# Kernel tuning notes

Measured on AMD Instinct MI355X. Metric: run time of the kernel, lower is better.

## Reference

```python
import jax, jax.numpy as jnp
import numpy as np

N_HEADS = 4
DIM_HEAD = 32
SCALE = DIM_HEAD ** -0.5
EPS = 1e-5


def setup_inputs() -> dict:
    key = jax.random.key(0)
    ks = jax.random.split(key, 5)
    b, dim, l, h, w = 8, 128, 32, 32, 32
    hidden = N_HEADS * DIM_HEAD  # 128
    return {
        "x": jax.random.normal(ks[0], (b, dim, l, h, w), dtype=jnp.float32),
        "w_qkv": jax.random.normal(ks[1], (3 * hidden, dim), dtype=jnp.float32) * 0.05,
        "w_out": jax.random.normal(ks[2], (dim, hidden), dtype=jnp.float32) * 0.05,
        "b_out": jax.random.normal(ks[3], (dim,), dtype=jnp.float32) * 0.05,
        "gn_gamma": jnp.ones((dim,), dtype=jnp.float32),
        "gn_beta": jnp.zeros((dim,), dtype=jnp.float32),
    }


def reference(x, w_qkv, w_out, b_out, gn_gamma, gn_beta):
    b, dim, l, h_sp, w_sp = x.shape
    n = l * h_sp * w_sp
    hidden = N_HEADS * DIM_HEAD
    xf = x.reshape(b, dim, n)  # flatten spatial -> tokens
    # 1x1 conv == channel matmul: [3*hidden, dim] x [b, dim, n]
    qkv = jnp.einsum('oc,bcn->bon', w_qkv, xf)
    qkv = qkv.reshape(b, 3, N_HEADS, DIM_HEAD, n)
    q, k, v = qkv[:, 0], qkv[:, 1], qkv[:, 2]  # each [b, H, d, n]
    q = jax.nn.softmax(q, axis=2) * SCALE      # softmax over feature dim d
    k = jax.nn.softmax(k, axis=-1)             # softmax over tokens n
    c = jnp.einsum('bhdn,bhen->bhde', k, v)    # [b, H, d, e] tiny context
    out = jnp.einsum('bhde,bhdn->bhen', c, q)  # [b, H, e, n]
    out = out.reshape(b, hidden, n)
    # to_out 1x1 conv + bias
    y = jnp.einsum('oc,bcn->bon', w_out, out) + b_out[None, :, None]
    # GroupNorm(1, dim): normalize over (C, spatial) per sample
    mean = jnp.mean(y, axis=(1, 2), keepdims=True)
    var = jnp.var(y, axis=(1, 2), keepdims=True)
    y = (y - mean) * jax.lax.rsqrt(var + EPS)
    y = y * gn_gamma[None, :, None] + gn_beta[None, :, None]
    return y.reshape(b, dim, l, h_sp, w_sp)
```

## Files before the change

### kernel.cpp

```cpp
#include <hip/hip_runtime.h>

#define BATCH 8
#define DIMC 128
#define NTOT 32768
#define HEADS 4
#define DHEAD 32
#define SCALE_Q 0.17677669529663687f
#define GRIDX 128
#define TILES 4

typedef _Float16 half8  __attribute__((ext_vector_type(8)));
typedef _Float16 half4v __attribute__((ext_vector_type(4)));
typedef _Float16 half2v __attribute__((ext_vector_type(2)));
typedef float    f32x4  __attribute__((ext_vector_type(4)));

#define WS_WQKV 0
#define WS_WOUT 98304
#define WS_S    131072
#define WS_Z    262144
#define WS_ST   266240
#define WS_CT   266304
#define WS_NEED 331840

__global__ void k0_prep(const float* __restrict__ wqkv, const float* __restrict__ wout,
                        char* __restrict__ ws) {
    int i = blockIdx.x * 256 + threadIdx.x;
    _Float16* Wb = (_Float16*)(ws + WS_WQKV);
    _Float16* Wo = (_Float16*)(ws + WS_WOUT);
    float* S  = (float*)(ws + WS_S);
    float* Z  = (float*)(ws + WS_Z);
    float* St = (float*)(ws + WS_ST);
    if (i < 49152) Wb[i] = (_Float16)wqkv[i];
    int j = i - 49152;
    if (j >= 0 && j < 16384) Wo[j] = (_Float16)wout[j];
    int k = j - 16384;
    if (k >= 0 && k < 32768) S[k] = 0.f;
    int m = k - 32768;
    if (m >= 0 && m < 1024) Z[m] = 0.f;
    int s = m - 1024;
    if (s >= 0 && s < 16) St[s] = 0.f;
}

__global__ __launch_bounds__(256, 2) void k1_kv(const float* __restrict__ x,
                                                const _Float16* __restrict__ Wb,
                                                float* __restrict__ S,
                                                float* __restrict__ Z) {
    __shared__ _Float16 Xb[64][136];
    __shared__ _Float16 KB[128][64];
    __shared__ _Float16 VB[128][64];
    const int t = threadIdx.x;
    const int lane = t & 63, w = t >> 6, g = lane >> 4, l15 = lane & 15;
    const int b = blockIdx.y;

    half8 af[4][4];
#pragma unroll
    for (int mt = 0; mt < 4; ++mt)
#pragma unroll
        for (int kc = 0; kc < 4; ++kc)
            af[mt][kc] = *(const half8*)(Wb + (size_t)(128 + (w * 4 + mt) * 16 + l15) * 128 + kc * 32 + 8 * g);

    f32x4 sacc[2][2];
#pragma unroll
    for (int dm = 0; dm < 2; ++dm)
#pragma unroll
        for (int en = 0; en < 2; ++en) sacc[dm][en] = (f32x4){0.f, 0.f, 0.f, 0.f};
    float zpart = 0.f;

    const int j4 = t & 15, c0 = t >> 4;
    const int sxw = (j4 & 7) << 3;

    float4 xr[8];
#pragma unroll
    for (int cc = 0; cc < 8; ++cc)
        xr[cc] = *(const float4*)(x + ((size_t)b * DIMC + c0 + 16 * cc) * NTOT + blockIdx.x * 64 + 4 * j4);
#pragma unroll
    for (int cc = 0; cc < 8; ++cc) {
        const int c = c0 + 16 * cc;
        Xb[4 * j4 + 0][c ^ sxw] = (_Float16)xr[cc].x;
        Xb[4 * j4 + 1][c ^ sxw] = (_Float16)xr[cc].y;
        Xb[4 * j4 + 2][c ^ sxw] = (_Float16)xr[cc].z;
        Xb[4 * j4 + 3][c ^ sxw] = (_Float16)xr[cc].w;
    }

    for (int it = 0; it < TILES; ++it) {
        if (it < TILES - 1) {
            const int j0n = (blockIdx.x + GRIDX * (it + 1)) * 64;
#pragma unroll
            for (int cc = 0; cc < 8; ++cc)
                xr[cc] = *(const float4*)(x + ((size_t)b * DIMC + c0 + 16 * cc) * NTOT + j0n + 4 * j4);
        }
        __syncthreads();
        half8 bf[4][4];
#pragma unroll
        for (int nt = 0; nt < 4; ++nt) {
            const int sb = ((4 * nt + (l15 >> 2)) & 7) << 3;
#pragma unroll
            for (int kc = 0; kc < 4; ++kc)
                bf[nt][kc] = *(const half8*)(&Xb[nt * 16 + l15][(kc * 32 + 8 * g) ^ sb]);
        }
#pragma unroll
        for (int mt = 0; mt < 4; ++mt) {
            f32x4 a0 = (f32x4){0.f,0.f,0.f,0.f}, a1 = a0, a2 = a0, a3 = a0;
#pragma unroll
            for (int kc = 0; kc < 4; ++kc) {
                a0 = __builtin_amdgcn_mfma_f32_16x16x32_f16(af[mt][kc], bf[0][kc], a0, 0, 0, 0);
                a1 = __builtin_amdgcn_mfma_f32_16x16x32_f16(af[mt][kc], bf[1][kc], a1, 0, 0, 0);
                a2 = __builtin_amdgcn_mfma_f32_16x16x32_f16(af[mt][kc], bf[2][kc], a2, 0, 0, 0);
                a3 = __builtin_amdgcn_mfma_f32_16x16x32_f16(af[mt][kc], bf[3][kc], a3, 0, 0, 0);
            }
            const int lr0 = (w * 4 + mt) * 16 + g * 4;
            const int skv = (((w * 4 + mt) * 4 + g) & 7) << 3;
#pragma unroll
            for (int nt = 0; nt < 4; ++nt) {
                const f32x4 a = (nt == 0) ? a0 : (nt == 1) ? a1 : (nt == 2) ? a2 : a3;
                const int jn = (nt * 16 + l15) ^ skv;
                if (lr0 < 128) {
#pragma unroll
                    for (int r = 0; r < 4; ++r) KB[lr0 + r][jn] = (_Float16)__expf(a[r]);
                } else {
#pragma unroll
                    for (int r = 0; r < 4; ++r) VB[lr0 - 128 + r][jn] = (_Float16)a[r];
                }
            }
        }
        __syncthreads();
        if (it < TILES - 1) {
#pragma unroll
            for (int cc = 0; cc < 8; ++cc) {
                const int c = c0 + 16 * cc;
                Xb[4 * j4 + 0][c ^ sxw] = (_Float16)xr[cc].x;
                Xb[4 * j4 + 1][c ^ sxw] = (_Float16)xr[cc].y;
                Xb[4 * j4 + 2][c ^ sxw] = (_Float16)xr[cc].z;
                Xb[4 * j4 + 3][c ^ sxw] = (_Float16)xr[cc].w;
            }
        }
#pragma unroll
        for (int dm = 0; dm < 2; ++dm) {
            const int sr = ((4 * dm + (l15 >> 2)) & 7) << 3;
#pragma unroll
            for (int en = 0; en < 2; ++en)
#pragma unroll
                for (int kc = 0; kc < 2; ++kc) {
                    half8 ka = *(const half8*)(&KB[w * 32 + dm * 16 + l15][(kc * 32 + 8 * g) ^ sr]);
                    half8 vb = *(const half8*)(&VB[w * 32 + en * 16 + l15][(kc * 32 + 8 * g) ^ sr]);
                    sacc[dm][en] = __builtin_amdgcn_mfma_f32_16x16x32_f16(ka, vb, sacc[dm][en], 0, 0, 0);
                }
        }
        {
            const int zr = lane >> 1;
            const int sz = ((zr >> 2) & 7) << 3;
#pragma unroll
            for (int s8 = 0; s8 < 4; ++s8) {
                half8 hv = *(const half8*)(&KB[w * 32 + zr][((lane & 1) * 32 + 8 * s8) ^ sz]);
#pragma unroll
                for (int e = 0; e < 8; ++e) zpart += (float)hv[e];
            }
        }
    }
    {
        float zt = zpart + __shfl_xor(zpart, 1);
        if ((lane & 1) == 0) atomicAdd(&Z[(b * HEADS + w) * DHEAD + (lane >> 1)], zt);
    }
#pragma unroll
    for (int dm = 0; dm < 2; ++dm)
#pragma unroll
        for (int en = 0; en < 2; ++en)
#pragma unroll
            for (int r = 0; r < 4; ++r)
                atomicAdd(&S[((size_t)(b * HEADS + w) * DHEAD + dm * 16 + g * 4 + r) * DHEAD + en * 16 + l15],
                          sacc[dm][en][r]);
}

__global__ void k2_ct(const float* __restrict__ S, const float* __restrict__ Z,
                      _Float16* __restrict__ CT) {
    int i = blockIdx.x * 256 + threadIdx.x;
    int d = i & 31, e = (i >> 5) & 31, bh = i >> 10;
    CT[i] = (_Float16)(S[(bh * 32 + d) * 32 + e] / Z[bh * 32 + d]);
}

__global__ __launch_bounds__(256, 2) void k3_main(const float* __restrict__ x,
                                                  const _Float16* __restrict__ Wb,
                                                  const _Float16* __restrict__ Wo,
                                                  const _Float16* __restrict__ CT,
                                                  const float* __restrict__ b_out,
                                                  char* __restrict__ ybase,
                                                  float* __restrict__ St) {
    __shared__ _Float16 Xb[64][136];
    __shared__ _Float16 qT[64][136];
    __shared__ _Float16 oT[64][136];
    __shared__ float scl[4][64];
    __shared__ float red[8];
    const int t = threadIdx.x;
    const int lane = t & 63, w = t >> 6, g = lane >> 4, l15 = lane & 15;
    const int b = blockIdx.y;
    const int j4 = t & 15, c0 = t >> 4;
    const int sxw = (j4 & 7) << 3;

    half8 wa[2][4];
#pragma unroll
    for (int mi = 0; mi < 2; ++mi)
#pragma unroll
        for (int kc = 0; kc < 4; ++kc)
            wa[mi][kc] = *(const half8*)(Wb + (size_t)((w * 2 + mi) * 16 + l15) * 128 + kc * 32 + 8 * g);
    half8 ca[2];
#pragma unroll
    for (int et = 0; et < 2; ++et)
        ca[et] = *(const half8*)(CT + ((size_t)(b * HEADS + w) * DHEAD + et * 16 + l15) * DHEAD + 8 * g);

    float ssum = 0.f, ssq = 0.f;

    float4 xr[8];
#pragma unroll
    for (int cc = 0; cc < 8; ++cc)
        xr[cc] = *(const float4*)(x + ((size_t)b * DIMC + c0 + 16 * cc) * NTOT + blockIdx.x * 64 + 4 * j4);
#pragma unroll
    for (int cc = 0; cc < 8; ++cc) {
        const int c = c0 + 16 * cc;
        Xb[4 * j4 + 0][c ^ sxw] = (_Float16)xr[cc].x;
        Xb[4 * j4 + 1][c ^ sxw] = (_Float16)xr[cc].y;
        Xb[4 * j4 + 2][c ^ sxw] = (_Float16)xr[cc].z;
        Xb[4 * j4 + 3][c ^ sxw] = (_Float16)xr[cc].w;
    }
    __syncthreads();

    for (int it = 0; it < TILES; ++it) {
        const int j0 = (blockIdx.x + GRIDX * it) * 64;
        if (it < TILES - 1) {
            const int j0n = (blockIdx.x + GRIDX * (it + 1)) * 64;
#pragma unroll
            for (int cc = 0; cc < 8; ++cc)
                xr[cc] = *(const float4*)(x + ((size_t)b * DIMC + c0 + 16 * cc) * NTOT + j0n + 4 * j4);
        }
        {
            half8 bf[4][4];
#pragma unroll
            for (int nt = 0; nt < 4; ++nt) {
                const int sb = ((4 * nt + (l15 >> 2)) & 7) << 3;
#pragma unroll
                for (int kc = 0; kc < 4; ++kc)
                    bf[nt][kc] = *(const half8*)(&Xb[nt * 16 + l15][(kc * 32 + 8 * g) ^ sb]);
            }
            float ps[4] = {0.f, 0.f, 0.f, 0.f};
#pragma unroll
            for (int mi = 0; mi < 2; ++mi) {
                const int mt = w * 2 + mi;
                f32x4 acc[4];
#pragma unroll
                for (int nt = 0; nt < 4; ++nt) acc[nt] = (f32x4){0.f, 0.f, 0.f, 0.f};
#pragma unroll
                for (int kc = 0; kc < 4; ++kc)
#pragma unroll
                    for (int nt = 0; nt < 4; ++nt)
                        acc[nt] = __builtin_amdgcn_mfma_f32_16x16x32_f16(wa[mi][kc], bf[nt][kc], acc[nt], 0, 0, 0);
#pragma unroll
                for (int nt = 0; nt < 4; ++nt) {
                    const int sb = ((4 * nt + (l15 >> 2)) & 7) << 3;
                    half4v p;
#pragma unroll
                    for (int r = 0; r < 4; ++r) {
                        const float e = __expf(acc[nt][r]);
                        ps[nt] += e;
                        p[r] = (_Float16)e;
                    }
                    *(half4v*)(&qT[nt * 16 + l15][(mt * 16 + g * 4) ^ sb]) = p;
                }
            }
#pragma unroll
            for (int nt = 0; nt < 4; ++nt) {
                ps[nt] += __shfl_xor(ps[nt], 16);
                ps[nt] += __shfl_xor(ps[nt], 32);
            }
            if (lane < 16) {
#pragma unroll
                for (int nt = 0; nt < 4; ++nt) scl[w][nt * 16 + lane] = SCALE_Q / ps[nt];
            }
        }
        __syncthreads();
        if (it < TILES - 1) {
#pragma unroll
            for (int cc = 0; cc < 8; ++cc) {
                const int c = c0 + 16 * cc;
                Xb[4 * j4 + 0][c ^ sxw] = (_Float16)xr[cc].x;
                Xb[4 * j4 + 1][c ^ sxw] = (_Float16)xr[cc].y;
                Xb[4 * j4 + 2][c ^ sxw] = (_Float16)xr[cc].z;
                Xb[4 * j4 + 3][c ^ sxw] = (_Float16)xr[cc].w;
            }
        }
        {
            half8 bf3[4];
            float sc[4];
#pragma unroll
            for (int nt = 0; nt < 4; ++nt) {
                const int sb = ((4 * nt + (l15 >> 2)) & 7) << 3;
                bf3[nt] = *(const half8*)(&qT[nt * 16 + l15][(w * 32 + 8 * g) ^ sb]);
                sc[nt] = scl[w][nt * 16 + l15];
            }
#pragma unroll
            for (int et = 0; et < 2; ++et) {
                f32x4 acc[4];
#pragma unroll
                for (int nt = 0; nt < 4; ++nt) acc[nt] = (f32x4){0.f, 0.f, 0.f, 0.f};
#pragma unroll
                for (int nt = 0; nt < 4; ++nt)
                    acc[nt] = __builtin_amdgcn_mfma_f32_16x16x32_f16(ca[et], bf3[nt], acc[nt], 0, 0, 0);
#pragma unroll
                for (int nt = 0; nt < 4; ++nt) {
                    const int sb = ((4 * nt + (l15 >> 2)) & 7) << 3;
                    half4v p;
#pragma unroll
                    for (int r = 0; r < 4; ++r) p[r] = (_Float16)(acc[nt][r] * sc[nt]);
                    *(half4v*)(&oT[nt * 16 + l15][(w * 32 + et * 16 + g * 4) ^ sb]) = p;
                }
            }
        }
        __syncthreads();
        {
            half8 bf[4][4];
#pragma unroll
            for (int nt = 0; nt < 4; ++nt) {
                const int sb = ((4 * nt + (l15 >> 2)) & 7) << 3;
#pragma unroll
                for (int kc = 0; kc < 4; ++kc)
                    bf[nt][kc] = *(const half8*)(&oT[nt * 16 + l15][(kc * 32 + 8 * g) ^ sb]);
            }
#pragma unroll
            for (int mi = 0; mi < 2; ++mi) {
                const int mt = w * 2 + mi;
                const int o0 = mt * 16 + g * 4;
                half8 af[4];
#pragma unroll
                for (int kc = 0; kc < 4; ++kc)
                    af[kc] = *(const half8*)(Wo + (size_t)(mt * 16 + l15) * 128 + kc * 32 + 8 * g);
                f32x4 acc[4];
#pragma unroll
                for (int nt = 0; nt < 4; ++nt) acc[nt] = (f32x4){0.f, 0.f, 0.f, 0.f};
#pragma unroll
                for (int kc = 0; kc < 4; ++kc)
#pragma unroll
                    for (int nt = 0; nt < 4; ++nt)
                        acc[nt] = __builtin_amdgcn_mfma_f32_16x16x32_f16(af[kc], bf[nt][kc], acc[nt], 0, 0, 0);
                float bo[4];
#pragma unroll
                for (int r = 0; r < 4; ++r) bo[r] = b_out[o0 + r];
#pragma unroll
                for (int r = 0; r < 4; ++r) {
                    _Float16* yrow = (_Float16*)(ybase + (size_t)(b * DIMC + o0 + r) * 131072 + 65536);
#pragma unroll
                    for (int nt = 0; nt < 4; ++nt) {
                        const int jn = j0 + nt * 16 + l15;
                        const float yv = acc[nt][r] + bo[r];
                        ssum += yv;
                        ssq += yv * yv;
                        yrow[jn] = (_Float16)yv;
                    }
                }
            }
        }
        __syncthreads();
    }
#pragma unroll
    for (int m = 32; m; m >>= 1) { ssum += __shfl_xor(ssum, m); ssq += __shfl_xor(ssq, m); }
    if (lane == 0) { red[w] = ssum; red[4 + w] = ssq; }
    __syncthreads();
    if (t == 0) {
        atomicAdd(&St[b * 2 + 0], red[0] + red[1] + red[2] + red[3]);
        atomicAdd(&St[b * 2 + 1], red[4] + red[5] + red[6] + red[7]);
    }
}

__global__ __launch_bounds__(256) void k4_norm(float* __restrict__ out, const float* __restrict__ St,
                                               const float* __restrict__ gamma,
                                               const float* __restrict__ beta) {
    const int o = blockIdx.x;
    const int b = blockIdx.y;
    const int t = threadIdx.x;
    const size_t row = (size_t)b * DIMC + o;
    const float n = (float)DIMC * (float)NTOT;
    const float mean = St[b * 2] / n;
    const float var = St[b * 2 + 1] / n - mean * mean;
    const float rs = rsqrtf(var + 1e-5f);
    const float ga = gamma[o] * rs;
    const float be = beta[o];
    const half8* yh = (const half8*)((const char*)out + row * 131072 + 65536);
    half8 hbuf[16];
#pragma unroll
    for (int i = 0; i < 16; ++i) hbuf[i] = yh[i * 256 + t];
    __syncthreads();
    float4* orow = (float4*)(out + row * NTOT);
#pragma unroll
    for (int i = 0; i < 16; ++i) {
        const int e4 = (i * 256 + t) * 2;
        float4 v0, v1;
        v0.x = ((float)hbuf[i][0] - mean) * ga + be;
        v0.y = ((float)hbuf[i][1] - mean) * ga + be;
        v0.z = ((float)hbuf[i][2] - mean) * ga + be;
        v0.w = ((float)hbuf[i][3] - mean) * ga + be;
        v1.x = ((float)hbuf[i][4] - mean) * ga + be;
        v1.y = ((float)hbuf[i][5] - mean) * ga + be;
        v1.z = ((float)hbuf[i][6] - mean) * ga + be;
        v1.w = ((float)hbuf[i][7] - mean) * ga + be;
        orow[e4] = v0;
        orow[e4 + 1] = v1;
    }
}

extern "C" void kernel_launch(void* const* d_in, const int* in_sizes, int n_in,
                              void* d_out, int out_size, void* d_ws, size_t ws_size,
                              hipStream_t stream) {
    const float* x     = (const float*)d_in[0];
    const float* wqkv  = (const float*)d_in[1];
    const float* wout  = (const float*)d_in[2];
    const float* b_out = (const float*)d_in[3];
    const float* gamma = (const float*)d_in[4];
    const float* beta  = (const float*)d_in[5];
    if (ws_size < WS_NEED) return;
    char* ws = (char*)d_ws;
    _Float16* Wb = (_Float16*)(ws + WS_WQKV);
    _Float16* Wo = (_Float16*)(ws + WS_WOUT);
    float* S  = (float*)(ws + WS_S);
    float* Z  = (float*)(ws + WS_Z);
    float* St = (float*)(ws + WS_ST);
    _Float16* CT = (_Float16*)(ws + WS_CT);

    k0_prep<<<389, 256, 0, stream>>>(wqkv, wout, ws);
    k1_kv<<<dim3(GRIDX, 8), 256, 0, stream>>>(x, Wb, S, Z);
    k2_ct<<<128, 256, 0, stream>>>(S, Z, CT);
    k3_main<<<dim3(GRIDX, 8), 256, 0, stream>>>(x, Wb, Wo, CT, b_out, (char*)d_out, St);
    k4_norm<<<dim3(128, 8), 256, 0, stream>>>((float*)d_out, St, gamma, beta);
}
```

Baseline: 153.7 us.

## Transpose x staging to per-token scalar loads with packed LDS writes, halve grid

The global-to-LDS staging of x in both the KV and main kernels changes from float4 loads along tokens to scalar loads where each thread owns one token and four consecutive channels. The four channels are packed into a single 8-byte half4 LDS store instead of four scattered 2-byte stores. This is meant to cut LDS store instructions and bank conflicts, while global loads stay coalesced across a wave. The grid in x is also halved and per-block tiles doubled, which lowers block count and amortizes the weight-fragment loads but reduces parallelism to 512 blocks.

```diff
diff --git a/kernel.cpp b/kernel.cpp
--- a/kernel.cpp
+++ b/kernel.cpp
@@ -6,8 +6,8 @@
 #define HEADS 4
 #define DHEAD 32
 #define SCALE_Q 0.17677669529663687f
-#define GRIDX 128
-#define TILES 4
+#define GRIDX 64
+#define TILES 8
 
 typedef _Float16 half8  __attribute__((ext_vector_type(8)));
 typedef _Float16 half4v __attribute__((ext_vector_type(4)));
@@ -41,6 +41,7 @@
     if (s >= 0 && s < 16) St[s] = 0.f;
 }
 
+
 __global__ __launch_bounds__(256, 2) void k1_kv(const float* __restrict__ x,
                                                 const _Float16* __restrict__ Wb,
                                                 float* __restrict__ S,
@@ -66,20 +67,19 @@
         for (int en = 0; en < 2; ++en) sacc[dm][en] = (f32x4){0.f, 0.f, 0.f, 0.f};
     float zpart = 0.f;
 
-    const int j4 = t & 15, c0 = t >> 4;
-    const int sxw = (j4 & 7) << 3;
-
-    float4 xr[8];
+    const int jt = t & 63, cq4 = (t >> 6) * 4;
+    const int sxw = ((jt >> 2) & 7) << 3;
+
+    float xr[8][4];
 #pragma unroll
     for (int cc = 0; cc < 8; ++cc)
-        xr[cc] = *(const float4*)(x + ((size_t)b * DIMC + c0 + 16 * cc) * NTOT + blockIdx.x * 64 + 4 * j4);
+#pragma unroll
+        for (int r = 0; r < 4; ++r)
+            xr[cc][r] = x[((size_t)b * DIMC + cq4 + 16 * cc + r) * NTOT + blockIdx.x * 64 + jt];
 #pragma unroll
     for (int cc = 0; cc < 8; ++cc) {
-        const int c = c0 + 16 * cc;
-        Xb[4 * j4 + 0][c ^ sxw] = (_Float16)xr[cc].x;
-        Xb[4 * j4 + 1][c ^ sxw] = (_Float16)xr[cc].y;
-        Xb[4 * j4 + 2][c ^ sxw] = (_Float16)xr[cc].z;
-        Xb[4 * j4 + 3][c ^ sxw] = (_Float16)xr[cc].w;
+        half4v p = {(_Float16)xr[cc][0], (_Float16)xr[cc][1], (_Float16)xr[cc][2], (_Float16)xr[cc][3]};
+        *(half4v*)(&Xb[jt][(cq4 + 16 * cc) ^ sxw]) = p;
     }
 
     for (int it = 0; it < TILES; ++it) {
@@ -87,7 +87,9 @@
             const int j0n = (blockIdx.x + GRIDX * (it + 1)) * 64;
 #pragma unroll
             for (int cc = 0; cc < 8; ++cc)
-                xr[cc] = *(const float4*)(x + ((size_t)b * DIMC + c0 + 16 * cc) * NTOT + j0n + 4 * j4);
+#pragma unroll
+                for (int r = 0; r < 4; ++r)
+                    xr[cc][r] = x[((size_t)b * DIMC + cq4 + 16 * cc + r) * NTOT + j0n + jt];
         }
         __syncthreads();
         half8 bf[4][4];
@@ -127,11 +129,8 @@
         if (it < TILES - 1) {
 #pragma unroll
             for (int cc = 0; cc < 8; ++cc) {
-                const int c = c0 + 16 * cc;
-                Xb[4 * j4 + 0][c ^ sxw] = (_Float16)xr[cc].x;
-                Xb[4 * j4 + 1][c ^ sxw] = (_Float16)xr[cc].y;
-                Xb[4 * j4 + 2][c ^ sxw] = (_Float16)xr[cc].z;
-                Xb[4 * j4 + 3][c ^ sxw] = (_Float16)xr[cc].w;
+                half4v p = {(_Float16)xr[cc][0], (_Float16)xr[cc][1], (_Float16)xr[cc][2], (_Float16)xr[cc][3]};
+                *(half4v*)(&Xb[jt][(cq4 + 16 * cc) ^ sxw]) = p;
             }
         }
 #pragma unroll
@@ -193,8 +192,8 @@
     const int t = threadIdx.x;
     const int lane = t & 63, w = t >> 6, g = lane >> 4, l15 = lane & 15;
     const int b = blockIdx.y;
-    const int j4 = t & 15, c0 = t >> 4;
-    const int sxw = (j4 & 7) << 3;
+    const int jt = t & 63, cq4 = (t >> 6) * 4;
+    const int sxw = ((jt >> 2) & 7) << 3;
 
     half8 wa[2][4];
 #pragma unroll
@@ -209,17 +208,16 @@
 
     float ssum = 0.f, ssq = 0.f;
 
-    float4 xr[8];
+    float xr[8][4];
 #pragma unroll
     for (int cc = 0; cc < 8; ++cc)
-        xr[cc] = *(const float4*)(x + ((size_t)b * DIMC + c0 + 16 * cc) * NTOT + blockIdx.x * 64 + 4 * j4);
+#pragma unroll
+        for (int r = 0; r < 4; ++r)
+            xr[cc][r] = x[((size_t)b * DIMC + cq4 + 16 * cc + r) * NTOT + blockIdx.x * 64 + jt];
 #pragma unroll
     for (int cc = 0; cc < 8; ++cc) {
-        const int c = c0 + 16 * cc;
-        Xb[4 * j4 + 0][c ^ sxw] = (_Float16)xr[cc].x;
-        Xb[4 * j4 + 1][c ^ sxw] = (_Float16)xr[cc].y;
-        Xb[4 * j4 + 2][c ^ sxw] = (_Float16)xr[cc].z;
-        Xb[4 * j4 + 3][c ^ sxw] = (_Float16)xr[cc].w;
+        half4v p = {(_Float16)xr[cc][0], (_Float16)xr[cc][1], (_Float16)xr[cc][2], (_Float16)xr[cc][3]};
+        *(half4v*)(&Xb[jt][(cq4 + 16 * cc) ^ sxw]) = p;
     }
     __syncthreads();
 
@@ -229,7 +227,9 @@
             const int j0n = (blockIdx.x + GRIDX * (it + 1)) * 64;
 #pragma unroll
             for (int cc = 0; cc < 8; ++cc)
-                xr[cc] = *(const float4*)(x + ((size_t)b * DIMC + c0 + 16 * cc) * NTOT + j0n + 4 * j4);
+#pragma unroll
+                for (int r = 0; r < 4; ++r)
+                    xr[cc][r] = x[((size_t)b * DIMC + cq4 + 16 * cc + r) * NTOT + j0n + jt];
         }
         {
             half8 bf[4][4];
@@ -279,11 +279,8 @@
         if (it < TILES - 1) {
 #pragma unroll
             for (int cc = 0; cc < 8; ++cc) {
-                const int c = c0 + 16 * cc;
-                Xb[4 * j4 + 0][c ^ sxw] = (_Float16)xr[cc].x;
-                Xb[4 * j4 + 1][c ^ sxw] = (_Float16)xr[cc].y;
-                Xb[4 * j4 + 2][c ^ sxw] = (_Float16)xr[cc].z;
-                Xb[4 * j4 + 3][c ^ sxw] = (_Float16)xr[cc].w;
+                half4v p = {(_Float16)xr[cc][0], (_Float16)xr[cc][1], (_Float16)xr[cc][2], (_Float16)xr[cc][3]};
+                *(half4v*)(&Xb[jt][(cq4 + 16 * cc) ^ sxw]) = p;
             }
         }
         {
```

After: 155.0 us. Within noise of the previous version (+0.8%).

## Fold per-head context into output projection weights, removing a GEMM stage

Applied to the files above, without the earlier changes.

A new small kernel premultiplies the output projection weights by the normalized per-head context matrices, giving a per-batch fused weight matrix G stored in a scratch slot of the output buffer. The main kernel then does one 128x128 MFMA GEMM on the scaled softmax of q instead of a context GEMM plus an output GEMM, which drops one LDS buffer, one barrier stage and the fp16 rounding of the intermediate. The q-softmax scale is now applied in registers before the LDS store. The grid is also halved with twice as many tiles per block, which lowers parallelism but amortizes the per-block setup, including loading the G fragments.

```diff
diff --git a/kernel.cpp b/kernel.cpp
--- a/kernel.cpp
+++ b/kernel.cpp
@@ -6,39 +6,33 @@
 #define HEADS 4
 #define DHEAD 32
 #define SCALE_Q 0.17677669529663687f
-#define GRIDX 128
-#define TILES 4
+#define GRIDX 64
+#define TILES 8
 
 typedef _Float16 half8  __attribute__((ext_vector_type(8)));
 typedef _Float16 half4v __attribute__((ext_vector_type(4)));
-typedef _Float16 half2v __attribute__((ext_vector_type(2)));
 typedef float    f32x4  __attribute__((ext_vector_type(4)));
 
 #define WS_WQKV 0
-#define WS_WOUT 98304
-#define WS_S    131072
-#define WS_Z    262144
-#define WS_ST   266240
-#define WS_CT   266304
-#define WS_NEED 331840
-
-__global__ void k0_prep(const float* __restrict__ wqkv, const float* __restrict__ wout,
-                        char* __restrict__ ws) {
+#define WS_S    98304
+#define WS_Z    229376
+#define WS_ST   233472
+#define WS_NEED 233536
+
+
+__global__ void k0_prep(const float* __restrict__ wqkv, char* __restrict__ ws) {
     int i = blockIdx.x * 256 + threadIdx.x;
     _Float16* Wb = (_Float16*)(ws + WS_WQKV);
-    _Float16* Wo = (_Float16*)(ws + WS_WOUT);
     float* S  = (float*)(ws + WS_S);
     float* Z  = (float*)(ws + WS_Z);
     float* St = (float*)(ws + WS_ST);
     if (i < 49152) Wb[i] = (_Float16)wqkv[i];
     int j = i - 49152;
-    if (j >= 0 && j < 16384) Wo[j] = (_Float16)wout[j];
-    int k = j - 16384;
-    if (k >= 0 && k < 32768) S[k] = 0.f;
-    int m = k - 32768;
-    if (m >= 0 && m < 1024) Z[m] = 0.f;
-    int s = m - 1024;
-    if (s >= 0 && s < 16) St[s] = 0.f;
+    if (j >= 0 && j < 32768) S[j] = 0.f;
+    int k = j - 32768;
+    if (k >= 0 && k < 1024) Z[k] = 0.f;
+    int m = k - 1024;
+    if (m >= 0 && m < 16) St[m] = 0.f;
 }
 
 __global__ __launch_bounds__(256, 2) void k1_kv(const float* __restrict__ x,
@@ -171,24 +165,40 @@
                           sacc[dm][en][r]);
 }
 
-__global__ void k2_ct(const float* __restrict__ S, const float* __restrict__ Z,
-                      _Float16* __restrict__ CT) {
-    int i = blockIdx.x * 256 + threadIdx.x;
-    int d = i & 31, e = (i >> 5) & 31, bh = i >> 10;
-    CT[i] = (_Float16)(S[(bh * 32 + d) * 32 + e] / Z[bh * 32 + d]);
+__global__ __launch_bounds__(256) void k2_g(const float* __restrict__ S, const float* __restrict__ Z,
+                                            const float* __restrict__ wout, char* __restrict__ ybase) {
+    __shared__ float Sd[32][33];
+    const int h = blockIdx.x, b = blockIdx.y;
+    const int t = threadIdx.x;
+    const float* Sb = S + (size_t)(b * HEADS + h) * 1024;
+    const float* Zb = Z + (size_t)(b * HEADS + h) * 32;
+    for (int i = t; i < 1024; i += 256) {
+        int d = i >> 5;
+        Sd[d][i & 31] = Sb[i] / Zb[d];
+    }
+    __syncthreads();
+    const int o = t & 127, dh = (t >> 7) * 16;
+    float wrow[32];
+#pragma unroll
+    for (int e = 0; e < 32; ++e) wrow[e] = wout[o * 128 + h * 32 + e];
+    _Float16* Gb = (_Float16*)(ybase + (size_t)(b >> 1) * 131072 + (size_t)(b & 1) * 32768);
+#pragma unroll
+    for (int dd = 0; dd < 16; ++dd) {
+        const int d = dh + dd;
+        float acc = 0.f;
+#pragma unroll
+        for (int e = 0; e < 32; ++e) acc = fmaf(wrow[e], Sd[d][e], acc);
+        Gb[o * 128 + h * 32 + d] = (_Float16)acc;
+    }
 }
 
 __global__ __launch_bounds__(256, 2) void k3_main(const float* __restrict__ x,
                                                   const _Float16* __restrict__ Wb,
-                                                  const _Float16* __restrict__ Wo,
-                                                  const _Float16* __restrict__ CT,
                                                   const float* __restrict__ b_out,
                                                   char* __restrict__ ybase,
                                                   float* __restrict__ St) {
     __shared__ _Float16 Xb[64][136];
     __shared__ _Float16 qT[64][136];
-    __shared__ _Float16 oT[64][136];
-    __shared__ float scl[4][64];
     __shared__ float red[8];
     const int t = threadIdx.x;
     const int lane = t & 63, w = t >> 6, g = lane >> 4, l15 = lane & 15;
@@ -197,15 +207,15 @@
     const int sxw = (j4 & 7) << 3;
 
     half8 wa[2][4];
+    half8 ga[2][4];
+    const _Float16* Gb = (const _Float16*)(ybase + (size_t)(b >> 1) * 131072 + (size_t)(b & 1) * 32768);
 #pragma unroll
     for (int mi = 0; mi < 2; ++mi)
 #pragma unroll
-        for (int kc = 0; kc < 4; ++kc)
+        for (int kc = 0; kc < 4; ++kc) {
             wa[mi][kc] = *(const half8*)(Wb + (size_t)((w * 2 + mi) * 16 + l15) * 128 + kc * 32 + 8 * g);
-    half8 ca[2];
-#pragma unroll
-    for (int et = 0; et < 2; ++et)
-        ca[et] = *(const half8*)(CT + ((size_t)(b * HEADS + w) * DHEAD + et * 16 + l15) * DHEAD + 8 * g);
+            ga[mi][kc] = *(const half8*)(Gb + (size_t)((w * 2 + mi) * 16 + l15) * 128 + kc * 32 + 8 * g);
+        }
 
     float ssum = 0.f, ssq = 0.f;
 
@@ -240,40 +250,46 @@
                 for (int kc = 0; kc < 4; ++kc)
                     bf[nt][kc] = *(const half8*)(&Xb[nt * 16 + l15][(kc * 32 + 8 * g) ^ sb]);
             }
+            f32x4 eacc[2][4];
+#pragma unroll
+            for (int mi = 0; mi < 2; ++mi)
+#pragma unroll
+                for (int nt = 0; nt < 4; ++nt) eacc[mi][nt] = (f32x4){0.f, 0.f, 0.f, 0.f};
+#pragma unroll
+            for (int mi = 0; mi < 2; ++mi)
+#pragma unroll
+                for (int kc = 0; kc < 4; ++kc)
+#pragma unroll
+                    for (int nt = 0; nt < 4; ++nt)
+                        eacc[mi][nt] = __builtin_amdgcn_mfma_f32_16x16x32_f16(wa[mi][kc], bf[nt][kc], eacc[mi][nt], 0, 0, 0);
             float ps[4] = {0.f, 0.f, 0.f, 0.f};
 #pragma unroll
-            for (int mi = 0; mi < 2; ++mi) {
-                const int mt = w * 2 + mi;
-                f32x4 acc[4];
-#pragma unroll
-                for (int nt = 0; nt < 4; ++nt) acc[nt] = (f32x4){0.f, 0.f, 0.f, 0.f};
-#pragma unroll
-                for (int kc = 0; kc < 4; ++kc)
-#pragma unroll
-                    for (int nt = 0; nt < 4; ++nt)
-                        acc[nt] = __builtin_amdgcn_mfma_f32_16x16x32_f16(wa[mi][kc], bf[nt][kc], acc[nt], 0, 0, 0);
+            for (int mi = 0; mi < 2; ++mi)
+#pragma unroll
+                for (int nt = 0; nt < 4; ++nt)
+#pragma unroll
+                    for (int r = 0; r < 4; ++r) {
+                        const float e = __expf(eacc[mi][nt][r]);
+                        ps[nt] += e;
+                        eacc[mi][nt][r] = e;
+                    }
+            float scn[4];
+#pragma unroll
+            for (int nt = 0; nt < 4; ++nt) {
+                ps[nt] += __shfl_xor(ps[nt], 16);
+                ps[nt] += __shfl_xor(ps[nt], 32);
+                scn[nt] = SCALE_Q / ps[nt];
+            }
+#pragma unroll
+            for (int mi = 0; mi < 2; ++mi)
 #pragma unroll
                 for (int nt = 0; nt < 4; ++nt) {
                     const int sb = ((4 * nt + (l15 >> 2)) & 7) << 3;
                     half4v p;
 #pragma unroll
-                    for (int r = 0; r < 4; ++r) {
-                        const float e = __expf(acc[nt][r]);
-                        ps[nt] += e;
-                        p[r] = (_Float16)e;
-                    }
-                    *(half4v*)(&qT[nt * 16 + l15][(mt * 16 + g * 4) ^ sb]) = p;
+                    for (int r = 0; r < 4; ++r) p[r] = (_Float16)(eacc[mi][nt][r] * scn[nt]);
+                    *(half4v*)(&qT[nt * 16 + l15][((w * 2 + mi) * 16 + g * 4) ^ sb]) = p;
                 }
-            }
-#pragma unroll
-            for (int nt = 0; nt < 4; ++nt) {
-                ps[nt] += __shfl_xor(ps[nt], 16);
-                ps[nt] += __shfl_xor(ps[nt], 32);
-            }
-            if (lane < 16) {
-#pragma unroll
-                for (int nt = 0; nt < 4; ++nt) scl[w][nt * 16 + lane] = SCALE_Q / ps[nt];
-            }
         }
         __syncthreads();
         if (it < TILES - 1) {
@@ -287,58 +303,25 @@
             }
         }
         {
-            half8 bf3[4];
-            float sc[4];
+            half8 bf[4][4];
 #pragma unroll
             for (int nt = 0; nt < 4; ++nt) {
                 const int sb = ((4 * nt + (l15 >> 2)) & 7) << 3;
-                bf3[nt] = *(const half8*)(&qT[nt * 16 + l15][(w * 32 + 8 * g) ^ sb]);
-                sc[nt] = scl[w][nt * 16 + l15];
-            }
-#pragma unroll
-            for (int et = 0; et < 2; ++et) {
+#pragma unroll
+                for (int kc = 0; kc < 4; ++kc)
+                    bf[nt][kc] = *(const half8*)(&qT[nt * 16 + l15][(kc * 32 + 8 * g) ^ sb]);
+            }
+#pragma unroll
+            for (int mi = 0; mi < 2; ++mi) {
+                const int o0 = (w * 2 + mi) * 16 + g * 4;
                 f32x4 acc[4];
 #pragma unroll
                 for (int nt = 0; nt < 4; ++nt) acc[nt] = (f32x4){0.f, 0.f, 0.f, 0.f};
 #pragma unroll
-                for (int nt = 0; nt < 4; ++nt)
-                    acc[nt] = __builtin_amdgcn_mfma_f32_16x16x32_f16(ca[et], bf3[nt], acc[nt], 0, 0, 0);
-#pragma unroll
-                for (int nt = 0; nt < 4; ++nt) {
-                    const int sb = ((4 * nt + (l15 >> 2)) & 7) << 3;
-                    half4v p;
-#pragma unroll
-                    for (int r = 0; r < 4; ++r) p[r] = (_Float16)(acc[nt][r] * sc[nt]);
-                    *(half4v*)(&oT[nt * 16 + l15][(w * 32 + et * 16 + g * 4) ^ sb]) = p;
-                }
-            }
-        }
-        __syncthreads();
-        {
-            half8 bf[4][4];
-#pragma unroll
-            for (int nt = 0; nt < 4; ++nt) {
-                const int sb = ((4 * nt + (l15 >> 2)) & 7) << 3;
-#pragma unroll
                 for (int kc = 0; kc < 4; ++kc)
-                    bf[nt][kc] = *(const half8*)(&oT[nt * 16 + l15][(kc * 32 + 8 * g) ^ sb]);
-            }
-#pragma unroll
-            for (int mi = 0; mi < 2; ++mi) {
-                const int mt = w * 2 + mi;
-                const int o0 = mt * 16 + g * 4;
-                half8 af[4];
-#pragma unroll
-                for (int kc = 0; kc < 4; ++kc)
-                    af[kc] = *(const half8*)(Wo + (size_t)(mt * 16 + l15) * 128 + kc * 32 + 8 * g);
-                f32x4 acc[4];
-#pragma unroll
-                for (int nt = 0; nt < 4; ++nt) acc[nt] = (f32x4){0.f, 0.f, 0.f, 0.f};
-#pragma unroll
-                for (int kc = 0; kc < 4; ++kc)
 #pragma unroll
                     for (int nt = 0; nt < 4; ++nt)
-                        acc[nt] = __builtin_amdgcn_mfma_f32_16x16x32_f16(af[kc], bf[nt][kc], acc[nt], 0, 0, 0);
+                        acc[nt] = __builtin_amdgcn_mfma_f32_16x16x32_f16(ga[mi][kc], bf[nt][kc], acc[nt], 0, 0, 0);
                 float bo[4];
 #pragma unroll
                 for (int r = 0; r < 4; ++r) bo[r] = b_out[o0 + r];
@@ -416,15 +399,13 @@
     if (ws_size < WS_NEED) return;
     char* ws = (char*)d_ws;
     _Float16* Wb = (_Float16*)(ws + WS_WQKV);
-    _Float16* Wo = (_Float16*)(ws + WS_WOUT);
     float* S  = (float*)(ws + WS_S);
     float* Z  = (float*)(ws + WS_Z);
     float* St = (float*)(ws + WS_ST);
-    _Float16* CT = (_Float16*)(ws + WS_CT);
-
-    k0_prep<<<389, 256, 0, stream>>>(wqkv, wout, ws);
+
+    k0_prep<<<325, 256, 0, stream>>>(wqkv, ws);
     k1_kv<<<dim3(GRIDX, 8), 256, 0, stream>>>(x, Wb, S, Z);
-    k2_ct<<<128, 256, 0, stream>>>(S, Z, CT);
-    k3_main<<<dim3(GRIDX, 8), 256, 0, stream>>>(x, Wb, Wo, CT, b_out, (char*)d_out, St);
+    k2_g<<<dim3(HEADS, 8), 256, 0, stream>>>(S, Z, wout, (char*)d_out);
+    k3_main<<<dim3(GRIDX, 8), 256, 0, stream>>>(x, Wb, b_out, (char*)d_out, St);
     k4_norm<<<dim3(128, 8), 256, 0, stream>>>((float*)d_out, St, gamma, beta);
 }
```

Measured after the change: 138.2 us. -10.1%, faster.
